# Kernel optimization log

Hardware: AMD Instinct MI355X
Metric: run time of the kernel (lower is better)

The kernel has to match this reference:

```python
import jax, jax.numpy as jnp
import numpy as np

D_MODEL = 1024
NUM_HEADS = 16
HEAD_DIM = D_MODEL // NUM_HEADS


def setup_inputs() -> dict:
    key = jax.random.key(0)
    kx, kq, kk, kv, ko = jax.random.split(key, 5)
    B, S = 2, 2048
    scale = 1.0 / np.sqrt(D_MODEL)
    return {
        "x": jax.random.normal(kx, (B, S, D_MODEL), dtype=jnp.float32),
        "W_q": jax.random.normal(kq, (D_MODEL, D_MODEL), dtype=jnp.float32) * scale,
        "W_k": jax.random.normal(kk, (D_MODEL, D_MODEL), dtype=jnp.float32) * scale,
        "W_v": jax.random.normal(kv, (D_MODEL, D_MODEL), dtype=jnp.float32) * scale,
        "W_o": jax.random.normal(ko, (D_MODEL, D_MODEL), dtype=jnp.float32) * scale,
        "causal": 1,
    }


def _attn(x, W_q, W_k, W_v, W_o, causal):
    B, S, D = x.shape
    H, Hd = NUM_HEADS, HEAD_DIM
    # projections: nn.Linear applies x @ W.T
    q = (x @ W_q.T).reshape(B, S, H, Hd)
    k = (x @ W_k.T).reshape(B, S, H, Hd)
    v = (x @ W_v.T).reshape(B, S, H, Hd)
    # scores: [B, H, S, S]
    scores = jnp.einsum("bqhd,bkhd->bhqk", q, k) / np.sqrt(Hd)
    if causal:
        mask = jnp.triu(jnp.ones((S, S), dtype=bool), k=1)
        scores = jnp.where(mask, -jnp.inf, scores)
    attn = jax.nn.softmax(scores, axis=-1)
    out = jnp.einsum("bhqk,bkhd->bqhd", attn, v).reshape(B, S, D)
    return out @ W_o.T


def reference(x, W_q, W_k, W_v, W_o, causal):
    return _attn(x, W_q, W_k, W_v, W_o, causal)
```

## Files before the change

kernel.cpp:

```cpp
#include <hip/hip_runtime.h>

typedef __attribute__((ext_vector_type(8))) short bf16x8;
typedef __attribute__((ext_vector_type(4))) float f32x4;
typedef __attribute__((ext_vector_type(4))) unsigned short u16x4;

#define MFMA16(a, b, c) __builtin_amdgcn_mfma_f32_16x16x32_bf16((a), (b), (c), 0, 0, 0)

static constexpr int D_MODEL = 1024;
static constexpr int SEQ = 2048;
static constexpr int NH = 16;
static constexpr int HD = 64;
static constexpr int LDA = 40;
static constexpr int MST = 136;
static constexpr float NEG_BIG = -1.0e30f;

__device__ __forceinline__ unsigned short f2bf(float f) {
  union { float f; unsigned int u; } v; v.f = f;
  unsigned int r = v.u + 0x7fffu + ((v.u >> 16) & 1u);
  return (unsigned short)(r >> 16);
}

__device__ __forceinline__ unsigned int cvtpk_bf16(float a, float b) {
  unsigned int r;
  asm("v_cvt_pk_bf16_f32 %0, %1, %2" : "=v"(r) : "v"(a), "v"(b));
  return r;
}

__device__ __forceinline__ bf16x8 ld8(const void* p, size_t eidx, int bf) {
  if (bf) return *(const bf16x8*)((const unsigned short*)p + eidx);
  const float* f = (const float*)p + eidx;
  f32x4 lo = *(const f32x4*)f;
  f32x4 hi = *(const f32x4*)(f + 4);
  bf16x8 r;
  r[0] = (short)f2bf(lo[0]); r[1] = (short)f2bf(lo[1]);
  r[2] = (short)f2bf(lo[2]); r[3] = (short)f2bf(lo[3]);
  r[4] = (short)f2bf(hi[0]); r[5] = (short)f2bf(hi[1]);
  r[6] = (short)f2bf(hi[2]); r[7] = (short)f2bf(hi[3]);
  return r;
}

__device__ __forceinline__ void async16(const unsigned short* g, unsigned short* l) {
  __builtin_amdgcn_global_load_lds(
      (const __attribute__((address_space(1))) void*)g,
      (__attribute__((address_space(3))) void*)l, 16, 0, 0);
}

__global__ __launch_bounds__(64) void detect_kernel(
    const unsigned short* __restrict__ xs, int* __restrict__ flag) {
  int lane = threadIdx.x;
  unsigned short s = xs[2 * lane];
  int e = (s >> 7) & 0xFF;
  bool hit = (e >= 117 && e <= 129);
  unsigned long long m = __ballot(hit);
  if (lane == 0) { flag[0] = (__popcll(m) >= 32) ? 1 : 0; flag[1] = 1; }
}

__global__ __launch_bounds__(256) void convert_kernel(
    const void* __restrict__ X,
    const void* __restrict__ W0, const void* __restrict__ W1,
    const void* __restrict__ W2, const void* __restrict__ W3,
    const int* __restrict__ flag,
    unsigned short* __restrict__ Xb, unsigned short* __restrict__ Wb)
{
  const int bf = *flag;
  const int ty = blockIdx.y;
  const void* src; unsigned short* dst; size_t n;
  if (ty == 0) { src = X; dst = Xb; n = (size_t)2 * SEQ * D_MODEL; }
  else {
    src = (ty == 1) ? W0 : (ty == 2) ? W1 : (ty == 3) ? W2 : W3;
    dst = Wb + (size_t)(ty - 1) * D_MODEL * D_MODEL;
    n = (size_t)D_MODEL * D_MODEL;
  }
  size_t i = ((size_t)blockIdx.x * 256 + threadIdx.x) * 8;
  if (i >= n) return;
  *(bf16x8*)(dst + i) = ld8(src, i, bf);
}

__device__ __forceinline__ void gemm_fast_core(
    const unsigned short* __restrict__ A, const unsigned short* __restrict__ B,
    int tm, int tn, unsigned short* smem, f32x4 acc[4][4])
{
  const int t = threadIdx.x;
  const int lane = t & 63;
  const int w = t >> 6;
  const int wm = (w >> 1) * 64, wn = (w & 1) * 64;
  const int quad = lane >> 4, l16 = lane & 15;
  const int srow = lane >> 2;
  const int scol = ((lane & 3) ^ ((lane >> 3) & 3)) * 8;
  const int xa = (l16 >> 1) & 3;

#pragma unroll
  for (int mi = 0; mi < 4; ++mi)
#pragma unroll
    for (int ni = 0; ni < 4; ++ni)
      acc[mi][ni] = (f32x4){0.f, 0.f, 0.f, 0.f};

  auto stage = [&](int f, int buf) {
    const int k0 = f * 32;
    unsigned short* dst = smem + buf * 8192;
#pragma unroll
    for (int i = 0; i < 2; ++i) {
      const int row = w * 32 + i * 16;
      async16(A + (size_t)(tm + row + srow) * D_MODEL + k0 + scol,
              dst + row * 32);
      async16(B + (size_t)(tn + row + srow) * D_MODEL + k0 + scol,
              dst + 4096 + row * 32);
    }
  };

  stage(0, 0);
  stage(1, 1);

  int cur = 0, nb = 2;
  for (int f = 0; f < 32; ++f) {
    if (f + 1 < 32) asm volatile("s_waitcnt vmcnt(4)" ::: "memory");
    else            asm volatile("s_waitcnt vmcnt(0)" ::: "memory");
    __builtin_amdgcn_s_barrier();
    __builtin_amdgcn_sched_barrier(0);
    if (f + 2 < 32) stage(f + 2, nb);
    const unsigned short* As = smem + cur * 8192;
    const unsigned short* Bs = As + 4096;
    bf16x8 af[4], bfv[4];
#pragma unroll
    for (int mi = 0; mi < 4; ++mi)
      af[mi] = *(const bf16x8*)(As + (wm + mi * 16 + l16) * 32 + (quad ^ xa) * 8);
#pragma unroll
    for (int ni = 0; ni < 4; ++ni)
      bfv[ni] = *(const bf16x8*)(Bs + (wn + ni * 16 + l16) * 32 + (quad ^ xa) * 8);
    __builtin_amdgcn_s_setprio(1);
#pragma unroll
    for (int mi = 0; mi < 4; ++mi)
#pragma unroll
      for (int ni = 0; ni < 4; ++ni)
        acc[mi][ni] = MFMA16(af[mi], bfv[ni], acc[mi][ni]);
    __builtin_amdgcn_s_setprio(0);
    cur = (cur == 2) ? 0 : cur + 1;
    nb = (nb == 2) ? 0 : nb + 1;
  }
}

__global__ __launch_bounds__(256) void qkv_fast_kernel(
    const unsigned short* __restrict__ X,
    const unsigned short* __restrict__ Wb,
    unsigned short* __restrict__ qd,
    unsigned short* __restrict__ kws,
    unsigned short* __restrict__ vws)
{
  __shared__ __align__(16) unsigned short smem[3 * 8192];
  const int bid = blockIdx.x;
  const int xcd = bid & 7, s0 = bid >> 3;
  const int tmg = xcd >> 2, tng = xcd & 3;
  const int tm_local = s0 / 6, zt = s0 % 6;
  const int z = zt >> 1, tn_local = zt & 1;
  const int tm = (tmg * 16 + tm_local) * 128;
  const int tn = (tng * 2 + tn_local) * 128;
  const unsigned short* W = Wb + (size_t)z * D_MODEL * D_MODEL;
  f32x4 acc[4][4];
  gemm_fast_core(X, W, tm, tn, smem, acc);

  const int t = threadIdx.x;
  const int lane = t & 63, w = t >> 6;
  const int wm = (w >> 1) * 64, wn = (w & 1) * 64;
  const int quad = lane >> 4, l16 = lane & 15;

  if (z == 2) {
    const int b = tm >> 11;
    const int sb = tm & 2047;
#pragma unroll
    for (int ph = 0; ph < 2; ++ph) {
      __syncthreads();
      if ((w & 1) == ph) {
#pragma unroll
        for (int mi = 0; mi < 4; ++mi)
#pragma unroll
          for (int ni = 0; ni < 4; ++ni)
#pragma unroll
            for (int r = 0; r < 4; ++r) {
              int m_local = wm + mi * 16 + quad * 4 + r;
              int n_sub = ni * 16 + l16;
              smem[n_sub * MST + m_local] = f2bf(acc[mi][ni][r]);
            }
      }
      __syncthreads();
      const int row = t >> 2, c0 = (t & 3) * 32;
      const int n_g = tn + ph * 64 + row;
      const int h = n_g >> 6, d = n_g & 63;
      unsigned short* dst = vws + (((size_t)b * NH + h) * HD + d) * SEQ + sb + c0;
#pragma unroll
      for (int cc = 0; cc < 4; ++cc)
        *(bf16x8*)(dst + cc * 8) = *(const bf16x8*)(smem + row * MST + c0 + cc * 8);
    }
    return;
  }
#pragma unroll
  for (int mi = 0; mi < 4; ++mi)
#pragma unroll
    for (int ni = 0; ni < 4; ++ni)
#pragma unroll
      for (int r = 0; r < 4; ++r) {
        int m = tm + wm + mi * 16 + quad * 4 + r;
        int n = tn + wn + ni * 16 + l16;
        unsigned short bv = f2bf(acc[mi][ni][r]);
        if (z == 0) {
          qd[(size_t)m * D_MODEL + n] = bv;
        } else {
          int b = m >> 11, sg = m & 2047;
          int h = n >> 6, d = n & 63;
          kws[(((size_t)b * NH + h) * SEQ + sg) * HD + d] = bv;
        }
      }
}

__global__ __launch_bounds__(256) void oproj_fast_kernel(
    const unsigned short* __restrict__ AW,
    const unsigned short* __restrict__ Wo,
    float* __restrict__ tmp)
{
  __shared__ __align__(16) unsigned short smem[3 * 8192];
  const int bid = blockIdx.x;
  const int xcd = bid & 7, s0 = bid >> 3;
  const int tmg = xcd >> 2, tng = xcd & 3;
  const int tm = (tmg * 16 + (s0 >> 1)) * 128;
  const int tn = (tng * 2 + (s0 & 1)) * 128;
  f32x4 acc[4][4];
  gemm_fast_core(AW, Wo, tm, tn, smem, acc);

  const int t = threadIdx.x;
  const int lane = t & 63, w = t >> 6;
  const int wm = (w >> 1) * 64, wn = (w & 1) * 64;
  const int quad = lane >> 4, l16 = lane & 15;
#pragma unroll
  for (int mi = 0; mi < 4; ++mi)
#pragma unroll
    for (int ni = 0; ni < 4; ++ni)
#pragma unroll
      for (int r = 0; r < 4; ++r) {
        int m = tm + wm + mi * 16 + quad * 4 + r;
        int n = tn + wn + ni * 16 + l16;
        tmp[(size_t)m * D_MODEL + n] = acc[mi][ni][r];
      }
}

__device__ __forceinline__ void gemm_tile_128x128(
    const void* __restrict__ A, const void* __restrict__ B, int bf,
    int tm, int tn, unsigned short* As, unsigned short* Bs, f32x4 acc[4][4])
{
  const int t = threadIdx.x;
  const int lane = t & 63;
  const int w = t >> 6;
  const int wm = (w >> 1) * 64, wn = (w & 1) * 64;
  const int quad = lane >> 4, l16 = lane & 15;
  const int r0 = t >> 2, kc = (t & 3) * 8;
  const int r1 = r0 + 64;

#pragma unroll
  for (int mi = 0; mi < 4; ++mi)
#pragma unroll
    for (int ni = 0; ni < 4; ++ni)
      acc[mi][ni] = (f32x4){0.f, 0.f, 0.f, 0.f};

  for (int k0 = 0; k0 < D_MODEL; k0 += 32) {
    bf16x8 a0 = ld8(A, (size_t)(tm + r0) * D_MODEL + k0 + kc, bf);
    bf16x8 a1 = ld8(A, (size_t)(tm + r1) * D_MODEL + k0 + kc, bf);
    bf16x8 b0 = ld8(B, (size_t)(tn + r0) * D_MODEL + k0 + kc, bf);
    bf16x8 b1 = ld8(B, (size_t)(tn + r1) * D_MODEL + k0 + kc, bf);
    __syncthreads();
    *(bf16x8*)(As + r0 * LDA + kc) = a0;
    *(bf16x8*)(As + r1 * LDA + kc) = a1;
    *(bf16x8*)(Bs + r0 * LDA + kc) = b0;
    *(bf16x8*)(Bs + r1 * LDA + kc) = b1;
    __syncthreads();
    bf16x8 af[4], bfv[4];
#pragma unroll
    for (int mi = 0; mi < 4; ++mi)
      af[mi] = *(const bf16x8*)(As + (wm + mi * 16 + l16) * LDA + quad * 8);
#pragma unroll
    for (int ni = 0; ni < 4; ++ni)
      bfv[ni] = *(const bf16x8*)(Bs + (wn + ni * 16 + l16) * LDA + quad * 8);
#pragma unroll
    for (int mi = 0; mi < 4; ++mi)
#pragma unroll
      for (int ni = 0; ni < 4; ++ni)
        acc[mi][ni] = MFMA16(af[mi], bfv[ni], acc[mi][ni]);
  }
}

__global__ __launch_bounds__(256) void qkv_kernel(
    const void* __restrict__ X,
    const void* __restrict__ Wq,
    const void* __restrict__ Wk,
    const void* __restrict__ Wv,
    const int* __restrict__ flag,
    unsigned short* __restrict__ qd,
    unsigned short* __restrict__ kws,
    unsigned short* __restrict__ vws)
{
  __shared__ __align__(16) unsigned short As[128 * LDA];
  __shared__ __align__(16) unsigned short Bs[128 * LDA];
  const int bf = *flag;
  const int z = blockIdx.z;
  const void* W = (z == 0) ? Wq : ((z == 1) ? Wk : Wv);
  const int tm = blockIdx.y * 128, tn = blockIdx.x * 128;
  f32x4 acc[4][4];
  gemm_tile_128x128(X, W, bf, tm, tn, As, Bs, acc);

  const int t = threadIdx.x;
  const int lane = t & 63, w = t >> 6;
  const int wm = (w >> 1) * 64, wn = (w & 1) * 64;
  const int quad = lane >> 4, l16 = lane & 15;
#pragma unroll
  for (int mi = 0; mi < 4; ++mi)
#pragma unroll
    for (int ni = 0; ni < 4; ++ni)
#pragma unroll
      for (int r = 0; r < 4; ++r) {
        int m = tm + wm + mi * 16 + quad * 4 + r;
        int n = tn + wn + ni * 16 + l16;
        unsigned short bv = f2bf(acc[mi][ni][r]);
        if (z == 0) {
          qd[(size_t)m * D_MODEL + n] = bv;
        } else {
          int b = m >> 11, s = m & 2047;
          int h = n >> 6, d = n & 63;
          if (z == 1) kws[(((size_t)b * NH + h) * SEQ + s) * HD + d] = bv;
          else        vws[(((size_t)b * NH + h) * HD + d) * SEQ + s] = bv;
        }
      }
}

__global__ __launch_bounds__(256) void oproj_kernel(
    const unsigned short* __restrict__ AW,
    const void* __restrict__ Wo,
    const int* __restrict__ flag,
    float* __restrict__ tmp)
{
  __shared__ __align__(16) unsigned short As[128 * LDA];
  __shared__ __align__(16) unsigned short Bs[128 * LDA];
  const int bf = *flag;
  const int t = threadIdx.x;
  const int lane = t & 63;
  const int w = t >> 6;
  const int wm = (w >> 1) * 64, wn = (w & 1) * 64;
  const int quad = lane >> 4, l16 = lane & 15;
  const int r0 = t >> 2, kc = (t & 3) * 8;
  const int r1 = r0 + 64;
  const int tm = blockIdx.y * 128, tn = blockIdx.x * 128;
  f32x4 acc[4][4];
#pragma unroll
  for (int mi = 0; mi < 4; ++mi)
#pragma unroll
    for (int ni = 0; ni < 4; ++ni)
      acc[mi][ni] = (f32x4){0.f, 0.f, 0.f, 0.f};

  for (int k0 = 0; k0 < D_MODEL; k0 += 32) {
    bf16x8 a0 = *(const bf16x8*)(AW + (size_t)(tm + r0) * D_MODEL + k0 + kc);
    bf16x8 a1 = *(const bf16x8*)(AW + (size_t)(tm + r1) * D_MODEL + k0 + kc);
    bf16x8 b0 = ld8(Wo, (size_t)(tn + r0) * D_MODEL + k0 + kc, bf);
    bf16x8 b1 = ld8(Wo, (size_t)(tn + r1) * D_MODEL + k0 + kc, bf);
    __syncthreads();
    *(bf16x8*)(As + r0 * LDA + kc) = a0;
    *(bf16x8*)(As + r1 * LDA + kc) = a1;
    *(bf16x8*)(Bs + r0 * LDA + kc) = b0;
    *(bf16x8*)(Bs + r1 * LDA + kc) = b1;
    __syncthreads();
    bf16x8 af[4], bfv[4];
#pragma unroll
    for (int mi = 0; mi < 4; ++mi)
      af[mi] = *(const bf16x8*)(As + (wm + mi * 16 + l16) * LDA + quad * 8);
#pragma unroll
    for (int ni = 0; ni < 4; ++ni)
      bfv[ni] = *(const bf16x8*)(Bs + (wn + ni * 16 + l16) * LDA + quad * 8);
#pragma unroll
    for (int mi = 0; mi < 4; ++mi)
#pragma unroll
      for (int ni = 0; ni < 4; ++ni)
        acc[mi][ni] = MFMA16(af[mi], bfv[ni], acc[mi][ni]);
  }
#pragma unroll
  for (int mi = 0; mi < 4; ++mi)
#pragma unroll
    for (int ni = 0; ni < 4; ++ni)
#pragma unroll
      for (int r = 0; r < 4; ++r) {
        int m = tm + wm + mi * 16 + quad * 4 + r;
        int n = tn + wn + ni * 16 + l16;
        tmp[(size_t)m * D_MODEL + n] = acc[mi][ni][r];
      }
}

__device__ __forceinline__ void qk_part(
    const bf16x8 (&kfr)[4][2], const bf16x8 (&aq)[2], f32x4 (&sc)[4])
{
  __builtin_amdgcn_s_setprio(1);
#pragma unroll
  for (int cb = 0; cb < 4; ++cb) {
    sc[cb] = (f32x4){0.f, 0.f, 0.f, 0.f};
    sc[cb] = MFMA16(kfr[cb][0], aq[0], sc[cb]);
    sc[cb] = MFMA16(kfr[cb][1], aq[1], sc[cb]);
  }
  __builtin_amdgcn_s_setprio(0);
}

__device__ __forceinline__ void smpv_part(
    f32x4 (&sc)[4], const bf16x8 (&vfr)[4][2], f32x4 (&oacc)[4], float& lsum,
    int diag, int ktbase, int qq, int quad, float Cs)
{
  if (diag) {
#pragma unroll
    for (int cb = 0; cb < 4; ++cb)
#pragma unroll
      for (int rr = 0; rr < 4; ++rr)
        if (ktbase + (cb & 1) * 32 + quad * 8 + (cb >> 1) * 4 + rr > qq)
          sc[cb][rr] = NEG_BIG;
  }
#pragma unroll
  for (int cb = 0; cb < 4; ++cb)
#pragma unroll
    for (int rr = 0; rr < 4; ++rr)
      sc[cb][rr] = __builtin_amdgcn_exp2f(sc[cb][rr] * Cs);
  f32x4 t0, t1;
#pragma unroll
  for (int rr = 0; rr < 4; ++rr) { t0[rr] = sc[0][rr] + sc[1][rr]; }
#pragma unroll
  for (int rr = 0; rr < 4; ++rr) { t1[rr] = sc[2][rr] + sc[3][rr]; }
#pragma unroll
  for (int rr = 0; rr < 4; ++rr) { t0[rr] += t1[rr]; }
  lsum += (t0[0] + t0[1]) + (t0[2] + t0[3]);
  bf16x8 bp[2];
#pragma unroll
  for (int hf = 0; hf < 2; ++hf) {
    union { unsigned int w4[4]; bf16x8 v; } u;
    u.w4[0] = cvtpk_bf16(sc[hf][0], sc[hf][1]);
    u.w4[1] = cvtpk_bf16(sc[hf][2], sc[hf][3]);
    u.w4[2] = cvtpk_bf16(sc[2 + hf][0], sc[2 + hf][1]);
    u.w4[3] = cvtpk_bf16(sc[2 + hf][2], sc[2 + hf][3]);
    bp[hf] = u.v;
  }
  __builtin_amdgcn_s_setprio(1);
#pragma unroll
  for (int db = 0; db < 4; ++db) {
    oacc[db] = MFMA16(vfr[db][0], bp[0], oacc[db]);
    oacc[db] = MFMA16(vfr[db][1], bp[1], oacc[db]);
  }
  __builtin_amdgcn_s_setprio(0);
}

__global__ __launch_bounds__(256, 2) void attn_kernel(
    unsigned short* __restrict__ Qd,
    const unsigned short* __restrict__ Kb,
    const unsigned short* __restrict__ Vt,
    const int* __restrict__ causal_p)
{
  __shared__ __align__(16) unsigned short Ks[3][64 * 64];
  __shared__ __align__(16) unsigned short Vs[3][64 * 64];
  const int bid = blockIdx.x;
  const int xcd = bid & 7, slot = bid >> 3;
  const int bhl = slot >> 4, p = slot & 15;
  const int bh = xcd * 4 + bhl;
  const int b = bh >> 4, h = bh & 15;
  const int t = threadIdx.x, lane = t & 63, w = t >> 6;
  const int quad = lane >> 4, l16 = lane & 15;
  const int causal = *causal_p;
  const int tA = causal ? (31 - p) : (2 * p);
  const int tB = causal ? p : (2 * p + 1);
  const int ITEMS = causal ? (32 - p) : 32;
  unsigned short* qh = Qd + (size_t)b * SEQ * D_MODEL + h * HD;
  const unsigned short* kh = Kb + ((size_t)b * NH + h) * SEQ * HD;
  const unsigned short* vh = Vt + ((size_t)b * NH + h) * HD * SEQ;
  const float Cs = 0.125f * 1.4426950408889634f;
  const int srow = lane >> 3;
  const int gcol = ((lane & 7) ^ srow) * 8;
  const int xa = l16 & 7;

  int kvp[2];
#pragma unroll
  for (int j2 = 0; j2 < 2; ++j2) {
    const int rp = w * 16 + j2 * 8 + srow;
    kvp[j2] = ((rp >> 4) & 1) * 32 + ((rp >> 2) & 3) * 8 + ((rp >> 5) & 1) * 4 + (rp & 3);
  }

  const int qA = tA * 64 + w * 16, qB = tB * 64 + w * 16;
  bf16x8 aqA[2], aqB[2];
#pragma unroll
  for (int ch = 0; ch < 2; ++ch) {
    aqA[ch] = *(const bf16x8*)(qh + (size_t)(qA + l16) * D_MODEL +
                               ch * 32 + quad * 8);
    aqB[ch] = *(const bf16x8*)(qh + (size_t)(qB + l16) * D_MODEL +
                               ch * 32 + quad * 8);
  }

  f32x4 oaccA[4], oaccB[4];
#pragma unroll
  for (int db = 0; db < 4; ++db) {
    oaccA[db] = (f32x4){0.f, 0.f, 0.f, 0.f};
    oaccB[db] = (f32x4){0.f, 0.f, 0.f, 0.f};
  }
  float lsumA = 0.f, lsumB = 0.f;

  auto stage = [&](int f, int buf) {
#pragma unroll
    for (int j2 = 0; j2 < 2; ++j2) {
      const int row = w * 16 + j2 * 8;
      async16(kh + (size_t)(f * 64 + kvp[j2]) * HD + gcol, &Ks[buf][row * 64]);
      async16(vh + (size_t)(row + srow) * SEQ + f * 64 + gcol, &Vs[buf][row * 64]);
    }
  };

  stage(0, 0);
  if (ITEMS > 1) stage(1, 1);

  int cur = 0, nb = 2;
  for (int f = 0; f < ITEMS; ++f) {
    if (f + 1 < ITEMS) asm volatile("s_waitcnt vmcnt(4)" ::: "memory");
    else               asm volatile("s_waitcnt vmcnt(0)" ::: "memory");
    __builtin_amdgcn_s_barrier();
    __builtin_amdgcn_sched_barrier(0);
    if (f + 2 < ITEMS) stage(f + 2, nb);

    bf16x8 kfr[4][2], vfr[4][2];
#pragma unroll
    for (int cb = 0; cb < 4; ++cb)
#pragma unroll
      for (int hf = 0; hf < 2; ++hf) {
        kfr[cb][hf] = *(const bf16x8*)(&Ks[cur][(cb * 16 + l16) * 64 +
                                               ((hf * 4 + quad) ^ xa) * 8]);
        vfr[cb][hf] = *(const bf16x8*)(&Vs[cur][(cb * 16 + l16) * 64 +
                                               ((hf * 4 + quad) ^ xa) * 8]);
      }
    const int bAct = causal ? (f <= p) : 1;
    f32x4 scA[4], scB[4];
    qk_part(kfr, aqA, scA);
    if (bAct) qk_part(kfr, aqB, scB);
    smpv_part(scA, vfr, oaccA, lsumA,
              causal && (f == ITEMS - 1), f * 64, qA + l16, quad, Cs);
    if (bAct)
      smpv_part(scB, vfr, oaccB, lsumB,
                causal && (f == p), f * 64, qB + l16, quad, Cs);
    cur = (cur == 2) ? 0 : cur + 1;
    nb = (nb == 2) ? 0 : nb + 1;
  }

  {
    float l = lsumA;
    l += __shfl_xor(l, 16, 64);
    l += __shfl_xor(l, 32, 64);
    float inv = 1.0f / l;
#pragma unroll
    for (int db = 0; db < 4; ++db) {
      u16x4 o;
#pragma unroll
      for (int rr = 0; rr < 4; ++rr) o[rr] = f2bf(oaccA[db][rr] * inv);
      *(u16x4*)(qh + (size_t)(qA + l16) * D_MODEL + db * 16 + quad * 4) = o;
    }
  }
  {
    float l = lsumB;
    l += __shfl_xor(l, 16, 64);
    l += __shfl_xor(l, 32, 64);
    float inv = 1.0f / l;
#pragma unroll
    for (int db = 0; db < 4; ++db) {
      u16x4 o;
#pragma unroll
      for (int rr = 0; rr < 4; ++rr) o[rr] = f2bf(oaccB[db][rr] * inv);
      *(u16x4*)(qh + (size_t)(qB + l16) * D_MODEL + db * 16 + quad * 4) = o;
    }
  }
}

__global__ __launch_bounds__(256) void final_kernel(
    const float* __restrict__ tmp, void* __restrict__ out,
    const int* __restrict__ flag)
{
  const int bf = *flag;
  size_t i = ((size_t)blockIdx.x * 256 + threadIdx.x) * 8;
  f32x4 lo = *(const f32x4*)(tmp + i);
  f32x4 hi = *(const f32x4*)(tmp + i + 4);
  if (bf) {
    bf16x8 r;
    r[0] = (short)f2bf(lo[0]); r[1] = (short)f2bf(lo[1]);
    r[2] = (short)f2bf(lo[2]); r[3] = (short)f2bf(lo[3]);
    r[4] = (short)f2bf(hi[0]); r[5] = (short)f2bf(hi[1]);
    r[6] = (short)f2bf(hi[2]); r[7] = (short)f2bf(hi[3]);
    *(bf16x8*)((unsigned short*)out + i) = r;
  } else {
    *(f32x4*)((float*)out + i) = lo;
    *(f32x4*)((float*)out + i + 4) = hi;
  }
}

extern "C" void kernel_launch(void* const* d_in, const int* in_sizes, int n_in,
                              void* d_out, int out_size, void* d_ws, size_t ws_size,
                              hipStream_t stream) {
  const void* X  = d_in[0];
  const void* Wq = d_in[1];
  const void* Wk = d_in[2];
  const void* Wv = d_in[3];
  const void* Wo = d_in[4];
  const int* causal = (const int*)d_in[5];

  const size_t NE = (size_t)2 * SEQ * D_MODEL;
  const size_t WE = (size_t)D_MODEL * D_MODEL;
  int* flag0 = (int*)d_ws;
  unsigned short* kws = (unsigned short*)((char*)d_ws + 64);
  unsigned short* vws = kws + NE;
  float* tmp = (float*)kws;
  unsigned short* Wb = vws + NE;
  unsigned short* qd = (unsigned short*)d_out;
  unsigned short* Xb = qd + NE;

  const bool big = ws_size >= (size_t)64 + 24ull * 1024 * 1024;

  hipLaunchKernelGGL(detect_kernel, dim3(1), dim3(64), 0, stream,
                     (const unsigned short*)X, flag0);
  if (big) {
    hipLaunchKernelGGL(convert_kernel, dim3(2048, 5), dim3(256), 0, stream,
                       X, Wq, Wk, Wv, Wo, flag0, Xb, Wb);
    hipLaunchKernelGGL(qkv_fast_kernel, dim3(768), dim3(256), 0, stream,
                       Xb, Wb, qd, kws, vws);
    hipLaunchKernelGGL(attn_kernel, dim3(512), dim3(256), 0, stream,
                       qd, kws, vws, causal);
    hipLaunchKernelGGL(oproj_fast_kernel, dim3(256), dim3(256), 0, stream,
                       qd, Wb + 3 * WE, tmp);
  } else {
    hipLaunchKernelGGL(qkv_kernel, dim3(8, 32, 3), dim3(256), 0, stream,
                       X, Wq, Wk, Wv, flag0, qd, kws, vws);
    hipLaunchKernelGGL(attn_kernel, dim3(512), dim3(256), 0, stream,
                       qd, kws, vws, causal);
    hipLaunchKernelGGL(oproj_kernel, dim3(8, 32), dim3(256), 0, stream,
                       qd, Wo, flag0, tmp);
  }
  hipLaunchKernelGGL(final_kernel, dim3(2048), dim3(256), 0, stream,
                     tmp, d_out, flag0);
}
```

Baseline: 181.5 us.

## Fold dtype detection into kernels, write output directly, remap block tiles

Removes the separate detect kernel and the final copy kernel on the large-workspace path. Each kernel now detects bf16 inputs inline, and the output projection writes straight to the result buffer in the correct dtype. Q and the bf16 copy of X move into a larger workspace, so the fast path needs 40MB instead of 24MB. The QKV block-to-tile mapping and the causal attention work-order per XCD are also changed to improve cache locality and load balance.

```diff
diff --git a/kernel.cpp b/kernel.cpp
--- a/kernel.cpp
+++ b/kernel.cpp
@@ -24,6 +24,14 @@
   unsigned int r;
   asm("v_cvt_pk_bf16_f32 %0, %1, %2" : "=v"(r) : "v"(a), "v"(b));
   return r;
+}
+
+__device__ __forceinline__ int detect_bf16(const unsigned short* xs, int lane) {
+  unsigned short s = xs[2 * lane];
+  int e = (s >> 7) & 0xFF;
+  bool hit = (e >= 117 && e <= 129);
+  unsigned long long m = __ballot(hit);
+  return (__popcll(m) >= 32) ? 1 : 0;
 }
 
 __device__ __forceinline__ bf16x8 ld8(const void* p, size_t eidx, int bf) {
@@ -59,10 +67,9 @@
     const void* __restrict__ X,
     const void* __restrict__ W0, const void* __restrict__ W1,
     const void* __restrict__ W2, const void* __restrict__ W3,
-    const int* __restrict__ flag,
     unsigned short* __restrict__ Xb, unsigned short* __restrict__ Wb)
 {
-  const int bf = *flag;
+  const int bf = detect_bf16((const unsigned short*)X, threadIdx.x & 63);
   const int ty = blockIdx.y;
   const void* src; unsigned short* dst; size_t n;
   if (ty == 0) { src = X; dst = Xb; n = (size_t)2 * SEQ * D_MODEL; }
@@ -149,11 +156,9 @@
   __shared__ __align__(16) unsigned short smem[3 * 8192];
   const int bid = blockIdx.x;
   const int xcd = bid & 7, s0 = bid >> 3;
-  const int tmg = xcd >> 2, tng = xcd & 3;
-  const int tm_local = s0 / 6, zt = s0 % 6;
-  const int z = zt >> 1, tn_local = zt & 1;
-  const int tm = (tmg * 16 + tm_local) * 128;
-  const int tn = (tng * 2 + tn_local) * 128;
+  const int z = s0 >> 5;
+  const int tn = ((s0 >> 2) & 7) * 128;
+  const int tm = (xcd * 4 + (s0 & 3)) * 128;
   const unsigned short* W = Wb + (size_t)z * D_MODEL * D_MODEL;
   f32x4 acc[4][4];
   gemm_fast_core(X, W, tm, tn, smem, acc);
@@ -214,9 +219,11 @@
 __global__ __launch_bounds__(256) void oproj_fast_kernel(
     const unsigned short* __restrict__ AW,
     const unsigned short* __restrict__ Wo,
-    float* __restrict__ tmp)
+    const unsigned short* __restrict__ Xorig,
+    void* __restrict__ out)
 {
   __shared__ __align__(16) unsigned short smem[3 * 8192];
+  const int bf = detect_bf16(Xorig, threadIdx.x & 63);
   const int bid = blockIdx.x;
   const int xcd = bid & 7, s0 = bid >> 3;
   const int tmg = xcd >> 2, tng = xcd & 3;
@@ -229,16 +236,31 @@
   const int lane = t & 63, w = t >> 6;
   const int wm = (w >> 1) * 64, wn = (w & 1) * 64;
   const int quad = lane >> 4, l16 = lane & 15;
-#pragma unroll
-  for (int mi = 0; mi < 4; ++mi)
-#pragma unroll
-    for (int ni = 0; ni < 4; ++ni)
-#pragma unroll
-      for (int r = 0; r < 4; ++r) {
-        int m = tm + wm + mi * 16 + quad * 4 + r;
-        int n = tn + wn + ni * 16 + l16;
-        tmp[(size_t)m * D_MODEL + n] = acc[mi][ni][r];
-      }
+  if (bf) {
+    unsigned short* o = (unsigned short*)out;
+#pragma unroll
+    for (int mi = 0; mi < 4; ++mi)
+#pragma unroll
+      for (int ni = 0; ni < 4; ++ni)
+#pragma unroll
+        for (int r = 0; r < 4; ++r) {
+          int m = tm + wm + mi * 16 + quad * 4 + r;
+          int n = tn + wn + ni * 16 + l16;
+          o[(size_t)m * D_MODEL + n] = f2bf(acc[mi][ni][r]);
+        }
+  } else {
+    float* o = (float*)out;
+#pragma unroll
+    for (int mi = 0; mi < 4; ++mi)
+#pragma unroll
+      for (int ni = 0; ni < 4; ++ni)
+#pragma unroll
+        for (int r = 0; r < 4; ++r) {
+          int m = tm + wm + mi * 16 + quad * 4 + r;
+          int n = tn + wn + ni * 16 + l16;
+          o[(size_t)m * D_MODEL + n] = acc[mi][ni][r];
+        }
+  }
 }
 
 __device__ __forceinline__ void gemm_tile_128x128(
@@ -455,7 +477,9 @@
   __shared__ __align__(16) unsigned short Vs[3][64 * 64];
   const int bid = blockIdx.x;
   const int xcd = bid & 7, slot = bid >> 3;
-  const int bhl = slot >> 4, p = slot & 15;
+  const int bhl = slot >> 4;
+  const int praw = slot & 15;
+  const int p = (bhl & 2) ? (15 - praw) : praw;
   const int bh = xcd * 4 + bhl;
   const int b = bh >> 4, h = bh & 15;
   const int t = threadIdx.x, lane = t & 63, w = t >> 6;
@@ -602,34 +626,36 @@
   const size_t NE = (size_t)2 * SEQ * D_MODEL;
   const size_t WE = (size_t)D_MODEL * D_MODEL;
   int* flag0 = (int*)d_ws;
+
   unsigned short* kws = (unsigned short*)((char*)d_ws + 64);
   unsigned short* vws = kws + NE;
-  float* tmp = (float*)kws;
-  unsigned short* Wb = vws + NE;
-  unsigned short* qd = (unsigned short*)d_out;
-  unsigned short* Xb = qd + NE;
-
-  const bool big = ws_size >= (size_t)64 + 24ull * 1024 * 1024;
-
-  hipLaunchKernelGGL(detect_kernel, dim3(1), dim3(64), 0, stream,
-                     (const unsigned short*)X, flag0);
+  unsigned short* Wb  = vws + NE;
+  unsigned short* qdf = Wb + 4 * WE;
+  unsigned short* Xbf = qdf + NE;
+
+  const bool big = ws_size >= (size_t)64 + 40ull * 1024 * 1024;
+
   if (big) {
     hipLaunchKernelGGL(convert_kernel, dim3(2048, 5), dim3(256), 0, stream,
-                       X, Wq, Wk, Wv, Wo, flag0, Xb, Wb);
+                       X, Wq, Wk, Wv, Wo, Xbf, Wb);
     hipLaunchKernelGGL(qkv_fast_kernel, dim3(768), dim3(256), 0, stream,
-                       Xb, Wb, qd, kws, vws);
+                       Xbf, Wb, qdf, kws, vws);
     hipLaunchKernelGGL(attn_kernel, dim3(512), dim3(256), 0, stream,
-                       qd, kws, vws, causal);
+                       qdf, kws, vws, causal);
     hipLaunchKernelGGL(oproj_fast_kernel, dim3(256), dim3(256), 0, stream,
-                       qd, Wb + 3 * WE, tmp);
+                       qdf, Wb + 3 * WE, (const unsigned short*)X, d_out);
   } else {
+    float* tmp = (float*)kws;
+    unsigned short* qd = (unsigned short*)d_out;
+    hipLaunchKernelGGL(detect_kernel, dim3(1), dim3(64), 0, stream,
+                       (const unsigned short*)X, flag0);
     hipLaunchKernelGGL(qkv_kernel, dim3(8, 32, 3), dim3(256), 0, stream,
                        X, Wq, Wk, Wv, flag0, qd, kws, vws);
     hipLaunchKernelGGL(attn_kernel, dim3(512), dim3(256), 0, stream,
                        qd, kws, vws, causal);
     hipLaunchKernelGGL(oproj_kernel, dim3(8, 32), dim3(256), 0, stream,
                        qd, Wo, flag0, tmp);
-  }
-  hipLaunchKernelGGL(final_kernel, dim3(2048), dim3(256), 0, stream,
-                     tmp, d_out, flag0);
-}
+    hipLaunchKernelGGL(final_kernel, dim3(2048), dim3(256), 0, stream,
+                       tmp, d_out, flag0);
+  }
+}
```

Result: faster. 172.1 us, median of 2 (-5.2%).
